# Optimization experiments

Hardware: AMD Instinct MI355X
Metric: run time of the kernel (lower is better)

Reference implementation:

```python
import jax, jax.numpy as jnp
import numpy as np

# Module constants from init_kwargs
TAU = 10.0
THR = 1.0
WIDTH_GRAD = 1.0   # beta of SingleExponential surrogate
SCALE_GRAD = 1.0   # grad_scale of SingleExponential surrogate
ALPHA = float(np.exp(-1.0 / TAU))  # leak factor used by both ExpLeak and LIF


@jax.custom_vjp
def spike(v):
    # sinabs SingleSpike: at most one spike per timestep
    return (v >= THR).astype(v.dtype)

def _spike_fwd(v):
    return spike(v), v

def _spike_bwd(v, g):
    # SingleExponential surrogate gradient
    return (g * SCALE_GRAD * jnp.exp(-WIDTH_GRAD * jnp.abs(v - THR)),)

spike.defvjp(_spike_fwd, _spike_bwd)


def setup_inputs() -> dict:
    key = jax.random.key(0)
    k1, k2 = jax.random.split(key)
    x = jax.random.normal(k1, (32768, 2, 4, 4, 100), dtype=jnp.float32)
    w = jax.random.normal(k2, (1, 32), dtype=jnp.float32)
    return {"x": x, "w": w}


def reference(x, w):
    # x: (B, 2, 4, 4, T); w: (1, 32) -- slayer dense = per-timestep linear 32 -> 1
    B, T = x.shape[0], x.shape[-1]
    xf = x.reshape(B, -1, T)                      # (B, 32, T)
    weighted = jnp.einsum('bft,of->bot', xf, w)   # (B, 1, T)
    i_seq = jnp.moveaxis(weighted, -1, 0)         # (T, B, 1) time-major for scan
    v0 = jnp.zeros_like(i_seq[0])

    # ExpLeak: v[t] = alpha * v[t-1] + i[t]
    def leak_step(v, i_t):
        v = ALPHA * v + i_t
        return v, v

    _, syn = jax.lax.scan(leak_step, v0, i_seq)   # (T, B, 1) synaptic currents

    # LIF (norm_input=True): v[t] = alpha*v[t-1] + (1-alpha)*i[t];
    # SingleSpike threshold crossing, MembraneSubtract reset.
    def lif_step(v, i_t):
        v = ALPHA * v + (1.0 - ALPHA) * i_t
        s = spike(v)
        return v - THR * s, s

    _, spikes = jax.lax.scan(lif_step, v0, syn)   # (T, B, 1)
    return jnp.moveaxis(spikes, 0, -1)            # (B, 1, T)
```

## Files before the change

### kernel.cpp

```cpp
#include <hip/hip_runtime.h>


typedef float vf4 __attribute__((ext_vector_type(4)));

constexpr int T_STEPS = 100;
constexpr int F_IN    = 32;
constexpr int NB      = 4;
constexpr int BLOCK   = 128;
constexpr int QT      = T_STEPS / 4;
constexpr int ROWF    = T_STEPS + 4;
constexpr int SLABF   = NB * F_IN * T_STEPS;
constexpr int CHUNKS  = SLABF / (4 * BLOCK);

__global__ __launch_bounds__(BLOCK) void snn_fused(
    const float* __restrict__ x,
    const float* __restrict__ w,
    float* __restrict__ out)
{
#pragma clang fp contract(off)
    __shared__ float xs[SLABF];
    __shared__ float cur[NB * ROWF];

    const int tid = threadIdx.x;
    const long long blk = blockIdx.x;
    const float* slab = x + blk * (long long)SLABF;

    vf4 v[CHUNKS];
#pragma unroll
    for (int c = 0; c < CHUNKS; ++c)
        v[c] = __builtin_nontemporal_load((const vf4*)slab + c * BLOCK + tid);
#pragma unroll
    for (int c = 0; c < CHUNKS; ++c)
        ((vf4*)xs)[c * BLOCK + tid] = v[c];

    float wf[F_IN];
#pragma unroll
    for (int f = 0; f < F_IN; ++f) wf[f] = w[f];

    __syncthreads();

    if (tid < NB * QT) {
        const int nb = tid / QT;
        const int j  = tid - nb * QT;
        const float* xr = xs + nb * (F_IN * T_STEPS) + 4 * j;
        float a0 = 0.0f, a1 = 0.0f, a2 = 0.0f, a3 = 0.0f;
#pragma unroll
        for (int f = 0; f < F_IN; ++f) {
            const vf4 xv = *(const vf4*)(xr + f * T_STEPS);
            a0 = a0 + xv.x * wf[f];
            a1 = a1 + xv.y * wf[f];
            a2 = a2 + xv.z * wf[f];
            a3 = a3 + xv.w * wf[f];
        }
        vf4* dst = (vf4*)(cur + nb * ROWF + 4 * j);
        *dst = vf4{a0, a1, a2, a3};
    }
    __syncthreads();

    if (tid < NB) {
        const double ALPHA64 = 0.90483741803595957316;
        const float  A   = (float)ALPHA64;
        const float  OMA = (float)(1.0 - ALPHA64);
        float syn = 0.0f, vmem = 0.0f;
        const float* row = cur + tid * ROWF;
        vf4* op = (vf4*)(out + (blk * NB + tid) * (long long)T_STEPS);
#pragma unroll
        for (int q = 0; q < QT; ++q) {
            vf4 s4;
#pragma unroll
            for (int k = 0; k < 4; ++k) {
                syn  = (A * syn) + row[4 * q + k];
                vmem = (A * vmem) + (OMA * syn);
                const float s = (vmem >= 1.0f) ? 1.0f : 0.0f;
                vmem = vmem - s;
                s4[k] = s;
            }
            op[q] = s4;
        }
    }
}

extern "C" void kernel_launch(void* const* d_in, const int* in_sizes, int n_in,
                              void* d_out, int out_size, void* d_ws, size_t ws_size,
                              hipStream_t stream) {
    const float* x  = (const float*)d_in[0];
    const float* w  = (const float*)d_in[1];
    float* out      = (float*)d_out;
    const int B       = in_sizes[0] / (F_IN * T_STEPS);
    const int nblocks = B / NB;
    snn_fused<<<nblocks, BLOCK, 0, stream>>>(x, w, out);
}
```

Before: 518.9 us.

## Split fused kernel into dense-projection and per-row scan kernels via workspace

```diff
diff --git a/kernel.cpp b/kernel.cpp
--- a/kernel.cpp
+++ b/kernel.cpp
@@ -12,9 +12,84 @@
 constexpr int SLABF   = NB * F_IN * T_STEPS;
 constexpr int CHUNKS  = SLABF / (4 * BLOCK);
 
-__global__ __launch_bounds__(BLOCK) void snn_fused(
+__global__ __launch_bounds__(BLOCK) void snn_dense(
     const float* __restrict__ x,
     const float* __restrict__ w,
+    float* __restrict__ cur_g)
+{
+#pragma clang fp contract(off)
+    __shared__ float xs[SLABF];
+
+    const int tid = threadIdx.x;
+    const long long blk = blockIdx.x;
+    const float* slab = x + blk * (long long)SLABF;
+
+    vf4 v[CHUNKS];
+#pragma unroll
+    for (int c = 0; c < CHUNKS; ++c)
+        v[c] = __builtin_nontemporal_load((const vf4*)slab + c * BLOCK + tid);
+#pragma unroll
+    for (int c = 0; c < CHUNKS; ++c)
+        ((vf4*)xs)[c * BLOCK + tid] = v[c];
+
+    float wf[F_IN];
+#pragma unroll
+    for (int f = 0; f < F_IN; ++f) wf[f] = w[f];
+
+    __syncthreads();
+
+    if (tid < NB * QT) {
+        const int nb = tid / QT;
+        const int j  = tid - nb * QT;
+        const float* xr = xs + nb * (F_IN * T_STEPS) + 4 * j;
+        float a0 = 0.0f, a1 = 0.0f, a2 = 0.0f, a3 = 0.0f;
+#pragma unroll
+        for (int f = 0; f < F_IN; ++f) {
+            const vf4 xv = *(const vf4*)(xr + f * T_STEPS);
+            a0 = a0 + xv.x * wf[f];
+            a1 = a1 + xv.y * wf[f];
+            a2 = a2 + xv.z * wf[f];
+            a3 = a3 + xv.w * wf[f];
+        }
+        vf4* dst = (vf4*)(cur_g + (blk * NB + nb) * (long long)T_STEPS + 4 * j);
+        *dst = vf4{a0, a1, a2, a3};
+    }
+}
+
+__global__ __launch_bounds__(BLOCK) void snn_scan(
+    const float* __restrict__ cur_g,
+    float* __restrict__ out)
+{
+#pragma clang fp contract(off)
+    const long long b = (long long)blockIdx.x * BLOCK + threadIdx.x;
+    const vf4* row = (const vf4*)(cur_g + b * (long long)T_STEPS);
+
+    vf4 rv[QT];
+#pragma unroll
+    for (int q = 0; q < QT; ++q) rv[q] = row[q];
+
+    const double ALPHA64 = 0.90483741803595957316;
+    const float  A   = (float)ALPHA64;
+    const float  OMA = (float)(1.0 - ALPHA64);
+    float syn = 0.0f, vmem = 0.0f;
+    vf4* op = (vf4*)(out + b * (long long)T_STEPS);
+#pragma unroll
+    for (int q = 0; q < QT; ++q) {
+        vf4 s4;
+#pragma unroll
+        for (int k = 0; k < 4; ++k) {
+            syn  = (A * syn) + rv[q][k];
+            vmem = (A * vmem) + (OMA * syn);
+            const float s = (vmem >= 1.0f) ? 1.0f : 0.0f;
+            vmem = vmem - s;
+            s4[k] = s;
+        }
+        op[q] = s4;
+    }
+}
+
+__global__ __launch_bounds__(BLOCK) void snn_fused(
+    const float* __restrict__ x, const float* __restrict__ w,
     float* __restrict__ out)
 {
 #pragma clang fp contract(off)
@@ -88,5 +163,13 @@
     float* out      = (float*)d_out;
     const int B       = in_sizes[0] / (F_IN * T_STEPS);
     const int nblocks = B / NB;
-    snn_fused<<<nblocks, BLOCK, 0, stream>>>(x, w, out);
+
+    const size_t cur_bytes = (size_t)B * T_STEPS * sizeof(float);
+    if (ws_size >= cur_bytes && d_ws != nullptr) {
+        float* cur_g = (float*)d_ws;
+        snn_dense<<<nblocks, BLOCK, 0, stream>>>(x, w, cur_g);
+        snn_scan<<<B / BLOCK, BLOCK, 0, stream>>>(cur_g, out);
+    } else {
+        snn_fused<<<nblocks, BLOCK, 0, stream>>>(x, w, out);
+    }
 }
```

Measured after the change: 523.5 us. No clear change (+0.9%).
